# Performance work log

Hardware: AMD Instinct MI355X
Metric: run time of the kernel (lower is better)

## Reference

```python
import jax, jax.numpy as jnp
import numpy as np

B, NC, A = 16, 80, 33600          # batch, num_classes, num_anchors
CLS_CH, REG_CH = 256, 256
TOPK_PRE, TOPK_POST = 750, 30
IOU_THRESH = 0.4                   # nms_thresh_val (module in eval mode)


def setup_inputs() -> dict:
    key = jax.random.key(0)
    k1, k2, k3, k4, k5 = jax.random.split(key, 5)
    # Build raw_preds so the first 4 channels are valid x1,y1,x2,y2 boxes
    xy = jax.random.uniform(k1, (B, 2, A)) * 600.0
    wh = jax.random.uniform(k2, (B, 2, A)) * 40.0 + 1.0
    boxes = jnp.concatenate([xy, xy + wh], axis=1)            # [B,4,A]
    cls_scores = jax.random.uniform(k3, (B, NC, A))            # sigmoid-like in [0,1)
    raw_preds = jnp.concatenate([boxes, cls_scores], axis=1).astype(jnp.float32)
    vid_features = jax.random.normal(k4, (B, A, CLS_CH), jnp.float32)
    reg_features = jax.random.normal(k5, (B, A, REG_CH), jnp.float32)
    return {"raw_preds": raw_preds, "vid_features": vid_features, "reg_features": reg_features}


def _nms_keep(boxes, cls_ids, iou_thresh):
    """torchvision.batched_nms: offset boxes per class so cross-class IoU == 0.
    boxes: [N,4] x1y1x2y2 sorted by descending score. Returns keep mask [N]."""
    max_coord = boxes.max()
    off = cls_ids.astype(boxes.dtype) * (max_coord + 1.0)
    b = boxes + off[:, None]
    x1, y1, x2, y2 = b[:, 0], b[:, 1], b[:, 2], b[:, 3]
    area = (x2 - x1) * (y2 - y1)
    iw = jnp.clip(jnp.minimum(x2[:, None], x2[None, :]) - jnp.maximum(x1[:, None], x1[None, :]), 0.0)
    ih = jnp.clip(jnp.minimum(y2[:, None], y2[None, :]) - jnp.maximum(y1[:, None], y1[None, :]), 0.0)
    inter = iw * ih
    iou = inter / (area[:, None] + area[None, :] - inter)     # [N,N]
    N = boxes.shape[0]
    idxs = jnp.arange(N)

    def body(i, keep):
        sup = keep[i] & (iou[i] > iou_thresh) & (idxs > i)
        return keep & jnp.logical_not(sup)

    return jax.lax.fori_loop(0, N, body, jnp.ones((N,), bool))


def _select_frame(boxes_b, max_scores_b, cls_ids_b):
    # top-k pre-NMS (sorted by descending score, like torch.topk)
    _, topk_idx = jax.lax.top_k(max_scores_b, TOPK_PRE)
    bsel = boxes_b[topk_idx]
    csel = cls_ids_b[topk_idx]
    keep = _nms_keep(bsel, csel, IOU_THRESH)
    # kept indices in score order; take first TOPK_POST (stable argsort: kept first)
    order = jnp.argsort(jnp.logical_not(keep))[:TOPK_POST]
    return topk_idx[order]                                    # [TOPK_POST]


def reference(raw_preds, vid_features, reg_features):
    preds = jnp.transpose(raw_preds, (0, 2, 1))               # [B,A,4+NC]
    boxes = preds[..., :4]
    scores = preds[..., 4:]
    max_scores = scores.max(axis=-1)                          # [B,A]
    cls_ids = jnp.argmax(scores, axis=-1)                     # [B,A]
    final_idx = jax.vmap(_select_frame)(boxes, max_scores, cls_ids)   # [B,TOPK_POST]

    gat = lambda f: jnp.take_along_axis(f, final_idx[..., None], axis=1)
    cls_f = gat(vid_features).reshape(1, -1, CLS_CH)          # [1,B*30,256]
    reg_f = gat(reg_features).reshape(1, -1, REG_CH)          # [1,B*30,256]
    box_f = gat(boxes).reshape(1, -1, 4)                      # [1,B*30,4]
    sc_f = jnp.take_along_axis(max_scores, final_idx, axis=1).reshape(1, -1)  # [1,B*30]
    return cls_f, reg_f, box_f, sc_f
```

## Files before the change

### kernel.cpp

```cpp
#include <hip/hip_runtime.h>
#include <stdint.h>

#pragma clang fp contract(off)

#define BB 16
#define NCC 80
#define AA 33600
#define A4 (AA / 4)
#define TOPK_PRE 750
#define TOPK_POST 30
#define NBINS 16384
#define CAND 1024

__global__ __launch_bounds__(256) void k_scoremax(const float* __restrict__ raw,
                                                  float* __restrict__ maxs,
                                                  int* __restrict__ clsid,
                                                  unsigned int* __restrict__ hist) {
  int gid = blockIdx.x * blockDim.x + threadIdx.x;
  if (gid >= BB * A4) return;
  int b = gid / A4, a4 = (gid - b * A4) * 4;
  const float* p = raw + (size_t)b * 84 * AA + (size_t)4 * AA + a4;
  float4 best = make_float4(-1e30f, -1e30f, -1e30f, -1e30f);
  int bc0 = 0, bc1 = 0, bc2 = 0, bc3 = 0;
  for (int c = 0; c < NCC; ++c) {
    float4 s = *(const float4*)(p + (size_t)c * AA);
    if (s.x > best.x) { best.x = s.x; bc0 = c; }
    if (s.y > best.y) { best.y = s.y; bc1 = c; }
    if (s.z > best.z) { best.z = s.z; bc2 = c; }
    if (s.w > best.w) { best.w = s.w; bc3 = c; }
  }
  *(float4*)(maxs + (size_t)b * AA + a4) = best;
  *(int4*)(clsid + (size_t)b * AA + a4) = make_int4(bc0, bc1, bc2, bc3);
  unsigned int* h = hist + b * NBINS;
  int d0 = 0x3F800000 - (int)__float_as_uint(best.x);
  int d1 = 0x3F800000 - (int)__float_as_uint(best.y);
  int d2 = 0x3F800000 - (int)__float_as_uint(best.z);
  int d3 = 0x3F800000 - (int)__float_as_uint(best.w);
  if (d0 >= 0 && d0 < NBINS - 1) atomicAdd(&h[d0], 1u);
  if (d1 >= 0 && d1 < NBINS - 1) atomicAdd(&h[d1], 1u);
  if (d2 >= 0 && d2 < NBINS - 1) atomicAdd(&h[d2], 1u);
  if (d3 >= 0 && d3 < NBINS - 1) atomicAdd(&h[d3], 1u);
}

__global__ __launch_bounds__(256) void k_selectnms(const float* __restrict__ maxs,
                                                   const int* __restrict__ clsid,
                                                   const unsigned int* __restrict__ hist,
                                                   const float* __restrict__ raw,
                                                   int* __restrict__ finalidx) {
  int b = blockIdx.x;
  int tid = threadIdx.x;
  __shared__ unsigned int psum[256];
  __shared__ unsigned int pref[256];
  __shared__ int s_cut;
  __shared__ unsigned int s_cnt0;
  __shared__ unsigned int keys[CAND];
  __shared__ float red[256];
  __shared__ float bx1[TOPK_PRE], by1[TOPK_PRE], bx2[TOPK_PRE], by2[TOPK_PRE], barea[TOPK_PRE];
  __shared__ int s_keep[TOPK_PRE];
  __shared__ int s_out[TOPK_POST];
  __shared__ int s_cnt;

  const unsigned int* h = hist + b * NBINS;
  unsigned int part = 0;
  for (int i = 0; i < 64; ++i) part += h[tid * 64 + i];
  psum[tid] = part;
  if (tid == 0) { s_cut = NBINS - 1; s_cnt0 = 0; s_cnt = 0; }
  __syncthreads();
  if (tid == 0) {
    unsigned int run = 0;
    for (int t = 0; t < 256; ++t) { pref[t] = run; run += psum[t]; }
  }
  __syncthreads();
  unsigned int base = pref[tid];
  if (base < TOPK_PRE && base + part >= TOPK_PRE) {
    unsigned int run = base;
    for (int i = 0; i < 64; ++i) {
      run += h[tid * 64 + i];
      if (run >= TOPK_PRE) { s_cut = tid * 64 + i; break; }
    }
  }
  for (int i = tid; i < CAND; i += 256) keys[i] = 0xFFFFFFFFu;
  __syncthreads();

  int cut = s_cut;
  for (int a = tid; a < AA; a += 256) {
    float v = maxs[(size_t)b * AA + a];
    int d = 0x3F800000 - (int)__float_as_uint(v);
    if (d >= 0 && d <= cut) {
      unsigned int pos = atomicAdd(&s_cnt0, 1u);
      if (pos < CAND) keys[pos] = ((unsigned int)d << 16) | (unsigned int)a;
    }
  }
  __syncthreads();

  for (int k = 2; k <= CAND; k <<= 1) {
    for (int j = k >> 1; j > 0; j >>= 1) {
      for (int s = tid; s < CAND; s += 256) {
        int p = s ^ j;
        if (p > s) {
          unsigned int x = keys[s], y = keys[p];
          bool up = ((s & k) == 0);
          if ((x > y) == up) { keys[s] = y; keys[p] = x; }
        }
      }
      __syncthreads();
    }
  }

  float lx1[3], ly1[3], lx2[3], ly2[3];
  int lcl[3];
  float m = -1e30f;
#pragma unroll
  for (int r = 0; r < 3; ++r) {
    int i = tid + r * 256;
    if (i < TOPK_PRE) {
      int a = (int)(keys[i] & 0xFFFFu);
      const float* p = raw + (size_t)b * 84 * AA + a;
      float x1 = p[0], y1 = p[AA], x2 = p[2 * AA], y2 = p[3 * AA];
      lx1[r] = x1; ly1[r] = y1; lx2[r] = x2; ly2[r] = y2;
      lcl[r] = clsid[(size_t)b * AA + a];
      m = fmaxf(m, fmaxf(fmaxf(x1, y1), fmaxf(x2, y2)));
    }
  }
  red[tid] = m;
  __syncthreads();
  for (int s = 128; s > 0; s >>= 1) {
    if (tid < s) red[tid] = fmaxf(red[tid], red[tid + s]);
    __syncthreads();
  }
  float mc1 = red[0] + 1.0f;
#pragma unroll
  for (int r = 0; r < 3; ++r) {
    int i = tid + r * 256;
    if (i < TOPK_PRE) {
      float off = (float)lcl[r] * mc1;
      float X1 = lx1[r] + off, Y1 = ly1[r] + off, X2 = lx2[r] + off, Y2 = ly2[r] + off;
      bx1[i] = X1; by1[i] = Y1; bx2[i] = X2; by2[i] = Y2;
      barea[i] = (X2 - X1) * (Y2 - Y1);
    }
  }
  for (int i = tid; i < TOPK_PRE; i += 256) s_keep[i] = 1;
  __syncthreads();

  for (int i = 0; i < TOPK_PRE; ++i) {
    if (s_keep[i]) {
      float X1 = bx1[i], Y1 = by1[i], X2 = bx2[i], Y2 = by2[i], Ai = barea[i];
      for (int j = i + 1 + tid; j < TOPK_PRE; j += 256) {
        float iw = fmaxf(fminf(X2, bx2[j]) - fmaxf(X1, bx1[j]), 0.0f);
        float ih = fmaxf(fminf(Y2, by2[j]) - fmaxf(Y1, by1[j]), 0.0f);
        float inter = iw * ih;
        float denom = (Ai + barea[j]) - inter;
        if (inter / denom > 0.4f) s_keep[j] = 0;
      }
      if (tid == 0) s_out[s_cnt++] = i;
      __syncthreads();
      if (s_cnt >= TOPK_POST) break;
    }
  }

  if (tid == 0) {
    int c = s_cnt;
    for (int j = 0; j < TOPK_PRE && c < TOPK_POST; ++j)
      if (!s_keep[j]) s_out[c++] = j;
  }
  __syncthreads();
  if (tid < TOPK_POST) finalidx[b * TOPK_POST + tid] = (int)(keys[s_out[tid]] & 0xFFFFu);
}

__global__ __launch_bounds__(256) void k_gather(const float* __restrict__ vid,
                                                const float* __restrict__ reg,
                                                const float* __restrict__ raw,
                                                const float* __restrict__ maxs,
                                                const int* __restrict__ finalidx,
                                                float* __restrict__ out) {
  int r = blockIdx.x;
  int b = r / TOPK_POST;
  int a = finalidx[r];
  int t = threadIdx.x;
  size_t src = ((size_t)b * AA + a) * 256 + t;
  out[(size_t)r * 256 + t] = vid[src];
  out[122880 + (size_t)r * 256 + t] = reg[src];
  if (t < 4) out[245760 + r * 4 + t] = raw[(size_t)b * 84 * AA + (size_t)t * AA + a];
  if (t == 4) out[247680 + r] = maxs[(size_t)b * AA + a];
}

extern "C" void kernel_launch(void* const* d_in, const int* in_sizes, int n_in,
                              void* d_out, int out_size, void* d_ws, size_t ws_size,
                              hipStream_t stream) {
  const float* raw = (const float*)d_in[0];
  const float* vid = (const float*)d_in[1];
  const float* reg = (const float*)d_in[2];
  float* out = (float*)d_out;

  char* ws = (char*)d_ws;
  size_t off = 0;
  auto alloc = [&](size_t nbytes) -> void* {
    void* p = ws + off;
    off = (off + nbytes + 255) & ~(size_t)255;
    return p;
  };
  float* maxs = (float*)alloc((size_t)BB * AA * 4);
  int* clsid = (int*)alloc((size_t)BB * AA * 4);
  unsigned int* hist = (unsigned int*)alloc((size_t)BB * NBINS * 4);
  int* finalidx = (int*)alloc((size_t)BB * TOPK_POST * 4);

  hipMemsetAsync(hist, 0, (size_t)BB * NBINS * 4, stream);

  k_scoremax<<<(BB * A4 + 255) / 256, 256, 0, stream>>>(raw, maxs, clsid, hist);
  k_selectnms<<<BB, 256, 0, stream>>>(maxs, clsid, hist, raw, finalidx);
  k_gather<<<BB * TOPK_POST, 256, 0, stream>>>(vid, reg, raw, maxs, finalidx, out);
}
```

Before: 1.004 ms.

## Compact top-score candidates in scoremax, drop full maxs/clsid arrays

The score-max kernel now packs each histogram-eligible anchor (score bin, anchor index, class id) into a 64-bit key and appends it to a per-batch candidate buffer using wave ballot plus one atomic per wave. This removes the full per-anchor max and class arrays. The select kernel then scans only the compacted candidates instead of all 33,600 anchors, with 512 threads and 64-bit sort keys. The final scores are decoded from the key, so the gather kernel no longer reads maxs. The cost is a capped candidate buffer (CAP 4096) that could drop candidates if too many anchors score near 1.0, plus a 64-bit bitonic sort.

```diff
diff --git a/kernel.cpp b/kernel.cpp
--- a/kernel.cpp
+++ b/kernel.cpp
@@ -11,14 +11,15 @@
 #define TOPK_POST 30
 #define NBINS 16384
 #define CAND 1024
+#define CAP 4096
 
 __global__ __launch_bounds__(256) void k_scoremax(const float* __restrict__ raw,
-                                                  float* __restrict__ maxs,
-                                                  int* __restrict__ clsid,
+                                                  unsigned long long* __restrict__ cand,
                                                   unsigned int* __restrict__ hist) {
-  int gid = blockIdx.x * blockDim.x + threadIdx.x;
-  if (gid >= BB * A4) return;
-  int b = gid / A4, a4 = (gid - b * A4) * 4;
+  int b = blockIdx.y;
+  int idx = blockIdx.x * 256 + threadIdx.x;
+  bool valid = (idx < A4);
+  int a4 = valid ? idx * 4 : (AA - 4);
   const float* p = raw + (size_t)b * 84 * AA + (size_t)4 * AA + a4;
   float4 best = make_float4(-1e30f, -1e30f, -1e30f, -1e30f);
   int bc0 = 0, bc1 = 0, bc2 = 0, bc3 = 0;
@@ -29,32 +30,48 @@
     if (s.z > best.z) { best.z = s.z; bc2 = c; }
     if (s.w > best.w) { best.w = s.w; bc3 = c; }
   }
-  *(float4*)(maxs + (size_t)b * AA + a4) = best;
-  *(int4*)(clsid + (size_t)b * AA + a4) = make_int4(bc0, bc1, bc2, bc3);
-  unsigned int* h = hist + b * NBINS;
-  int d0 = 0x3F800000 - (int)__float_as_uint(best.x);
-  int d1 = 0x3F800000 - (int)__float_as_uint(best.y);
-  int d2 = 0x3F800000 - (int)__float_as_uint(best.z);
-  int d3 = 0x3F800000 - (int)__float_as_uint(best.w);
-  if (d0 >= 0 && d0 < NBINS - 1) atomicAdd(&h[d0], 1u);
-  if (d1 >= 0 && d1 < NBINS - 1) atomicAdd(&h[d1], 1u);
-  if (d2 >= 0 && d2 < NBINS - 1) atomicAdd(&h[d2], 1u);
-  if (d3 >= 0 && d3 < NBINS - 1) atomicAdd(&h[d3], 1u);
-}
-
-__global__ __launch_bounds__(256) void k_selectnms(const float* __restrict__ maxs,
-                                                   const int* __restrict__ clsid,
+  unsigned int* hb = hist + b * NBINS;
+  unsigned int* cnt = hist + (size_t)BB * NBINS;
+  unsigned long long* cb = cand + (size_t)b * CAP;
+  int lane = threadIdx.x & 63;
+  float vs[4] = {best.x, best.y, best.z, best.w};
+  int cs[4] = {bc0, bc1, bc2, bc3};
+#pragma unroll
+  for (int k = 0; k < 4; ++k) {
+    int d = 0x3F800000 - (int)__float_as_uint(vs[k]);
+    bool want = valid && (d >= 0) && (d < NBINS - 1);
+    unsigned long long mask = __ballot(want);
+    if (want) atomicAdd(&hb[d], 1u);
+    int n = __popcll(mask);
+    if (n) {
+      unsigned int base = 0u;
+      int leader = __ffsll((unsigned long long)mask) - 1;
+      if (lane == leader) base = atomicAdd(&cnt[b], (unsigned int)n);
+      base = __shfl(base, leader, 64);
+      if (want) {
+        unsigned int pos = base + (unsigned int)__popcll(mask & ((1ull << lane) - 1ull));
+        if (pos < CAP)
+          cb[pos] = ((unsigned long long)(unsigned int)d << 23) |
+                    ((unsigned long long)(unsigned int)(a4 + k) << 7) |
+                    (unsigned long long)(unsigned int)cs[k];
+      }
+    }
+  }
+}
+
+__global__ __launch_bounds__(512) void k_selectnms(const unsigned long long* __restrict__ cand,
                                                    const unsigned int* __restrict__ hist,
                                                    const float* __restrict__ raw,
-                                                   int* __restrict__ finalidx) {
+                                                   int* __restrict__ finalidx,
+                                                   float* __restrict__ finalscore) {
   int b = blockIdx.x;
   int tid = threadIdx.x;
-  __shared__ unsigned int psum[256];
-  __shared__ unsigned int pref[256];
+  __shared__ unsigned int psum[512];
+  __shared__ unsigned int pref[512];
   __shared__ int s_cut;
   __shared__ unsigned int s_cnt0;
-  __shared__ unsigned int keys[CAND];
-  __shared__ float red[256];
+  __shared__ unsigned long long keys[CAND];
+  __shared__ float red[512];
   __shared__ float bx1[TOPK_PRE], by1[TOPK_PRE], bx2[TOPK_PRE], by2[TOPK_PRE], barea[TOPK_PRE];
   __shared__ int s_keep[TOPK_PRE];
   __shared__ int s_out[TOPK_POST];
@@ -62,43 +79,45 @@
 
   const unsigned int* h = hist + b * NBINS;
   unsigned int part = 0;
-  for (int i = 0; i < 64; ++i) part += h[tid * 64 + i];
+  for (int i = 0; i < 32; ++i) part += h[tid * 32 + i];
   psum[tid] = part;
   if (tid == 0) { s_cut = NBINS - 1; s_cnt0 = 0; s_cnt = 0; }
   __syncthreads();
   if (tid == 0) {
     unsigned int run = 0;
-    for (int t = 0; t < 256; ++t) { pref[t] = run; run += psum[t]; }
+    for (int t = 0; t < 512; ++t) { pref[t] = run; run += psum[t]; }
   }
   __syncthreads();
   unsigned int base = pref[tid];
   if (base < TOPK_PRE && base + part >= TOPK_PRE) {
     unsigned int run = base;
-    for (int i = 0; i < 64; ++i) {
-      run += h[tid * 64 + i];
-      if (run >= TOPK_PRE) { s_cut = tid * 64 + i; break; }
-    }
-  }
-  for (int i = tid; i < CAND; i += 256) keys[i] = 0xFFFFFFFFu;
+    for (int i = 0; i < 32; ++i) {
+      run += h[tid * 32 + i];
+      if (run >= TOPK_PRE) { s_cut = tid * 32 + i; break; }
+    }
+  }
+  for (int i = tid; i < CAND; i += 512) keys[i] = ~0ull;
   __syncthreads();
 
   int cut = s_cut;
-  for (int a = tid; a < AA; a += 256) {
-    float v = maxs[(size_t)b * AA + a];
-    int d = 0x3F800000 - (int)__float_as_uint(v);
-    if (d >= 0 && d <= cut) {
+  unsigned int n = hist[(size_t)BB * NBINS + b];
+  if (n > CAP) n = CAP;
+  for (unsigned int i = tid; i < n; i += 512) {
+    unsigned long long key = cand[(size_t)b * CAP + i];
+    int d = (int)(key >> 23);
+    if (d <= cut) {
       unsigned int pos = atomicAdd(&s_cnt0, 1u);
-      if (pos < CAND) keys[pos] = ((unsigned int)d << 16) | (unsigned int)a;
+      if (pos < CAND) keys[pos] = key;
     }
   }
   __syncthreads();
 
   for (int k = 2; k <= CAND; k <<= 1) {
     for (int j = k >> 1; j > 0; j >>= 1) {
-      for (int s = tid; s < CAND; s += 256) {
+      for (int s = tid; s < CAND; s += 512) {
         int p = s ^ j;
         if (p > s) {
-          unsigned int x = keys[s], y = keys[p];
+          unsigned long long x = keys[s], y = keys[p];
           bool up = ((s & k) == 0);
           if ((x > y) == up) { keys[s] = y; keys[p] = x; }
         }
@@ -107,31 +126,32 @@
     }
   }
 
-  float lx1[3], ly1[3], lx2[3], ly2[3];
-  int lcl[3];
+  float lx1[2], ly1[2], lx2[2], ly2[2];
+  int lcl[2];
   float m = -1e30f;
 #pragma unroll
-  for (int r = 0; r < 3; ++r) {
-    int i = tid + r * 256;
+  for (int r = 0; r < 2; ++r) {
+    int i = tid + r * 512;
     if (i < TOPK_PRE) {
-      int a = (int)(keys[i] & 0xFFFFu);
+      unsigned long long key = keys[i];
+      int a = (int)((key >> 7) & 0xFFFFu);
       const float* p = raw + (size_t)b * 84 * AA + a;
       float x1 = p[0], y1 = p[AA], x2 = p[2 * AA], y2 = p[3 * AA];
       lx1[r] = x1; ly1[r] = y1; lx2[r] = x2; ly2[r] = y2;
-      lcl[r] = clsid[(size_t)b * AA + a];
+      lcl[r] = (int)(key & 0x7Fu);
       m = fmaxf(m, fmaxf(fmaxf(x1, y1), fmaxf(x2, y2)));
     }
   }
   red[tid] = m;
   __syncthreads();
-  for (int s = 128; s > 0; s >>= 1) {
+  for (int s = 256; s > 0; s >>= 1) {
     if (tid < s) red[tid] = fmaxf(red[tid], red[tid + s]);
     __syncthreads();
   }
   float mc1 = red[0] + 1.0f;
 #pragma unroll
-  for (int r = 0; r < 3; ++r) {
-    int i = tid + r * 256;
+  for (int r = 0; r < 2; ++r) {
+    int i = tid + r * 512;
     if (i < TOPK_PRE) {
       float off = (float)lcl[r] * mc1;
       float X1 = lx1[r] + off, Y1 = ly1[r] + off, X2 = lx2[r] + off, Y2 = ly2[r] + off;
@@ -139,13 +159,13 @@
       barea[i] = (X2 - X1) * (Y2 - Y1);
     }
   }
-  for (int i = tid; i < TOPK_PRE; i += 256) s_keep[i] = 1;
+  for (int i = tid; i < TOPK_PRE; i += 512) s_keep[i] = 1;
   __syncthreads();
 
   for (int i = 0; i < TOPK_PRE; ++i) {
     if (s_keep[i]) {
       float X1 = bx1[i], Y1 = by1[i], X2 = bx2[i], Y2 = by2[i], Ai = barea[i];
-      for (int j = i + 1 + tid; j < TOPK_PRE; j += 256) {
+      for (int j = i + 1 + tid; j < TOPK_PRE; j += 512) {
         float iw = fmaxf(fminf(X2, bx2[j]) - fmaxf(X1, bx1[j]), 0.0f);
         float ih = fmaxf(fminf(Y2, by2[j]) - fmaxf(Y1, by1[j]), 0.0f);
         float inter = iw * ih;
@@ -164,13 +184,17 @@
       if (!s_keep[j]) s_out[c++] = j;
   }
   __syncthreads();
-  if (tid < TOPK_POST) finalidx[b * TOPK_POST + tid] = (int)(keys[s_out[tid]] & 0xFFFFu);
+  if (tid < TOPK_POST) {
+    unsigned long long key = keys[s_out[tid]];
+    finalidx[b * TOPK_POST + tid] = (int)((key >> 7) & 0xFFFFu);
+    finalscore[b * TOPK_POST + tid] = __uint_as_float(0x3F800000u - (unsigned int)(key >> 23));
+  }
 }
 
 __global__ __launch_bounds__(256) void k_gather(const float* __restrict__ vid,
                                                 const float* __restrict__ reg,
                                                 const float* __restrict__ raw,
-                                                const float* __restrict__ maxs,
+                                                const float* __restrict__ finalscore,
                                                 const int* __restrict__ finalidx,
                                                 float* __restrict__ out) {
   int r = blockIdx.x;
@@ -181,7 +205,7 @@
   out[(size_t)r * 256 + t] = vid[src];
   out[122880 + (size_t)r * 256 + t] = reg[src];
   if (t < 4) out[245760 + r * 4 + t] = raw[(size_t)b * 84 * AA + (size_t)t * AA + a];
-  if (t == 4) out[247680 + r] = maxs[(size_t)b * AA + a];
+  if (t == 4) out[247680 + r] = finalscore[r];
 }
 
 extern "C" void kernel_launch(void* const* d_in, const int* in_sizes, int n_in,
@@ -199,14 +223,15 @@
     off = (off + nbytes + 255) & ~(size_t)255;
     return p;
   };
-  float* maxs = (float*)alloc((size_t)BB * AA * 4);
-  int* clsid = (int*)alloc((size_t)BB * AA * 4);
-  unsigned int* hist = (unsigned int*)alloc((size_t)BB * NBINS * 4);
+  unsigned int* hist = (unsigned int*)alloc((size_t)BB * NBINS * 4 + (size_t)BB * 4);
+  unsigned long long* cand = (unsigned long long*)alloc((size_t)BB * CAP * 8);
   int* finalidx = (int*)alloc((size_t)BB * TOPK_POST * 4);
-
-  hipMemsetAsync(hist, 0, (size_t)BB * NBINS * 4, stream);
-
-  k_scoremax<<<(BB * A4 + 255) / 256, 256, 0, stream>>>(raw, maxs, clsid, hist);
-  k_selectnms<<<BB, 256, 0, stream>>>(maxs, clsid, hist, raw, finalidx);
-  k_gather<<<BB * TOPK_POST, 256, 0, stream>>>(vid, reg, raw, maxs, finalidx, out);
-}
+  float* finalscore = (float*)alloc((size_t)BB * TOPK_POST * 4);
+
+  hipMemsetAsync(hist, 0, (size_t)BB * NBINS * 4 + (size_t)BB * 4, stream);
+
+  dim3 gA((A4 + 255) / 256, BB);
+  k_scoremax<<<gA, 256, 0, stream>>>(raw, cand, hist);
+  k_selectnms<<<BB, 512, 0, stream>>>(cand, hist, raw, finalidx, finalscore);
+  k_gather<<<BB * TOPK_POST, 256, 0, stream>>>(vid, reg, raw, finalscore, finalidx, out);
+}
```

Result: slower. 1.030 ms (+2.6%).
